# Optimization experiments

Hardware: AMD Instinct MI355X
Metric: run time of the kernel (lower is better)

The kernel has to match this reference:

```python
import jax, jax.numpy as jnp
import numpy as np

K = 16  # neighbors per point (init kwarg k)


def setup_inputs() -> dict:
    key = jax.random.key(0)
    k0, k1, k2 = jax.random.split(key, 3)
    B, N, C, L, O = 4, 8192, 32, 64, 128
    return {
        "x": jax.random.normal(k0, (B, N, C), dtype=jnp.float32),
        "W_lin": jax.random.normal(k1, (C, L), dtype=jnp.float32) * 0.1,
        "b_lin": jnp.zeros((L,), dtype=jnp.float32),
        "W_conv": jax.random.normal(k2, (L, O), dtype=jnp.float32) * 0.1,
        "b_conv": jnp.zeros((O,), dtype=jnp.float32),
    }


def reference(x, W_lin, b_lin, W_conv, b_conv):
    # --- knn(x, k): squared-euclidean pairwise distance + top-k nearest ---
    sq = jnp.sum(x * x, axis=-1)                                   # [B,N]
    # dist[b,i,j] = ||x_i - x_j||^2  (self included, dist 0)
    dist = sq[:, :, None] - 2.0 * jnp.einsum('bnc,bmc->bnm', x, x) + sq[:, None, :]
    _, idx = jax.lax.top_k(-dist, K)                               # [B,N,K] int32
    # --- index_points: gather neighbor features ---
    knn_x = jax.vmap(lambda xb, ib: xb[ib])(x, idx)                # [B,N,K,C]
    # --- max pool over neighbors ---
    pooled = jnp.max(knn_x, axis=2)                                # [B,N,C]
    # --- Dense(linear) -> Conv1D(out_channel, kernel_size=1) -> relu ---
    h = pooled @ W_lin + b_lin                                     # [B,N,64]
    h = h @ W_conv + b_conv                                        # [B,N,128]
    return jax.nn.relu(h)
```

## Files before the change

### kernel.cpp

```cpp
#include <hip/hip_runtime.h>

#define NPTS   8192
#define CCH    32
#define LDIM   64
#define ODIM   128
#define KNN    16
#define QPB    64
#define TILEC  128
#define NTIL   (NPTS / TILEC)
#define NBLK   ((4 * NPTS) / QPB)
#define SCAP   57
#define MARGIN 0.75f
#define T32STR 65

typedef _Float16 half8   __attribute__((ext_vector_type(8)));
typedef float    float4v __attribute__((ext_vector_type(4)));

#define LDS_BYTES 54016
#define OFF_SQ   8192
#define OFF_SL   34816
#define OFF_SC   49408
#define OFF_TQ   49664
#define OFF_KN   49920
#define OFF_HH   8704

__device__ __forceinline__ void gload_lds16(const void* g, void* l) {
    __builtin_amdgcn_global_load_lds(
        (const __attribute__((address_space(1))) unsigned int*)g,
        (__attribute__((address_space(3))) unsigned int*)l, 16, 0, 0);
}
__device__ __forceinline__ void gload_lds4(const void* g, void* l) {
    __builtin_amdgcn_global_load_lds(
        (const __attribute__((address_space(1))) unsigned int*)g,
        (__attribute__((address_space(3))) unsigned int*)l, 4, 0, 0);
}

__global__ void prep_kernel(const float* __restrict__ x, float* __restrict__ sqg,
                            _Float16* __restrict__ xh) {
    int p = blockIdx.x * 256 + threadIdx.x;
    const float4* src = (const float4*)(x + (size_t)p * CCH);
    float4 f[8];
    #pragma unroll
    for (int k = 0; k < 8; ++k) f[k] = src[k];
    float s = 0.f;
    #pragma unroll
    for (int k = 0; k < 8; ++k)
        s += f[k].x * f[k].x + f[k].y * f[k].y + f[k].z * f[k].z + f[k].w * f[k].w;
    sqg[p] = s;
    half8* dst = (half8*)xh + ((p >> 7) * 512 + ((p >> 4) & 7) * 64 + (p & 15));
    #pragma unroll
    for (int q = 0; q < 4; ++q) {
        float4 a = f[2 * q], c = f[2 * q + 1];
        half8 h;
        h[0] = (_Float16)a.x; h[1] = (_Float16)a.y; h[2] = (_Float16)a.z; h[3] = (_Float16)a.w;
        h[4] = (_Float16)c.x; h[5] = (_Float16)c.y; h[6] = (_Float16)c.z; h[7] = (_Float16)c.w;
        dst[q * 16] = h;
    }
}

__global__ __launch_bounds__(512, 4)
void graph_layer_kernel(const float* __restrict__ x,
                        const float* __restrict__ sqg,
                        const _Float16* __restrict__ xh,
                        const float* __restrict__ Wl,
                        const float* __restrict__ bl,
                        const float* __restrict__ Wc,
                        const float* __restrict__ bc,
                        float* __restrict__ out)
{
    __shared__ __align__(16) char smem[LDS_BYTES];
    int*   slist = (int*)(smem + OFF_SL);
    float* t32   = (float*)smem;
    int*   scnt  = (int*)(smem + OFF_SC);
    float* tq    = (float*)(smem + OFF_TQ);
    float* skeys = (float*)smem;
    int*   kn    = (int*)(smem + OFF_KN);
    float* pl    = (float*)smem;
    float* hh    = (float*)(smem + OFF_HH);

    const int tid  = threadIdx.x;
    const int lane = tid & 63;
    const int w    = tid >> 6;
    const int g    = w >> 2;
    const int lw   = w & 3;
    const int col  = lane & 15;
    const int quad = lane >> 4;
    const float INF = __builtin_inff();

    const int qb0 = blockIdx.x * QPB;
    const int b   = qb0 >> 13;
    const int qbl = qb0 & (NPTS - 1);
    const int S   = blockIdx.x & 31;
    const float* xb  = x   + (size_t)(b << 13) * CCH;
    const float* sqb = sqg + (b << 13);
    const char*  xhb = (const char*)xh + (size_t)b * NTIL * 8192;

    half8 qh;
    {
        int p = qb0 + lw * 16 + col;
        qh = *(const half8*)((const char*)xh
              + (size_t)(p >> 7) * 8192 + ((p >> 4) & 7) * 1024
              + quad * 256 + (p & 15) * 16);
    }

    auto tileof = [&](int I) { return (((I + S) & 31) << 1) | g; };
    auto bufat  = [&](int I) { return smem + (((g << 1) | (I & 1)) * 8704); };

    auto stage = [&](int I) {
        char* sb = bufat(I);
        int tile = tileof(I);
        const char* src = xhb + (size_t)tile * 8192;
        int tg = tid & 255;
        gload_lds16(src + tg * 16,        sb + lw * 1024);
        gload_lds16(src + 4096 + tg * 16, sb + 4096 + lw * 1024);
        if (lw < 2)
            gload_lds4(sqb + tile * TILEC + lw * 64 + lane, sb + OFF_SQ + lw * 256);
    };

    float m1[4] = {INF, INF, INF, INF};
    float m2[4] = {INF, INF, INF, INF};

    stage(0);
    __syncthreads();
    #pragma unroll 1
    for (int I = 0; I < 32; ++I) {
        if (I + 1 < 32) stage(I + 1);
        const char*  cb = bufat(I);
        const float* sv = (const float*)(cb + OFF_SQ);
        #pragma unroll
        for (int st = 0; st < 8; ++st) {
            half8 bh = *(const half8*)(cb + st * 1024 + lane * 16);
            float sc = sv[st * 16 + col];
            float4v acc = __builtin_amdgcn_mfma_f32_16x16x32_f16(
                qh, bh, (float4v){0.f, 0.f, 0.f, 0.f}, 0, 0, 0);
            #pragma unroll
            for (int j = 0; j < 4; ++j) {
                float key = fmaf(-2.f, acc[j], sc);
                float o1  = m1[j];
                m1[j] = fminf(key, o1);
                m2[j] = __builtin_amdgcn_fmed3f(key, o1, m2[j]);
            }
        }
        __syncthreads();
    }

    #pragma unroll
    for (int j = 0; j < 4; ++j) {
        int qq = lw * 16 + quad * 4 + j;
        t32[qq * T32STR + g * 32 + col * 2 + 0] = m1[j];
        t32[qq * T32STR + g * 32 + col * 2 + 1] = m2[j];
    }
    __syncthreads();
    {
        int q  = tid & 63;
        int wt = tid >> 6;
        float v[8]; int r[8];
        #pragma unroll
        for (int u = 0; u < 8; ++u) { v[u] = t32[q * T32STR + wt * 8 + u]; r[u] = 0; }
        #pragma unroll 8
        for (int jj = 0; jj < 64; ++jj) {
            float vj = t32[q * T32STR + jj];
            #pragma unroll
            for (int u = 0; u < 8; ++u)
                r[u] += (int)(vj < v[u]) | ((int)(vj == v[u]) & (int)(jj < wt * 8 + u));
        }
        #pragma unroll
        for (int u = 0; u < 8; ++u)
            if (r[u] == KNN - 1) tq[q] = v[u];
        if (tid < QPB) scnt[tid] = 0;
    }
    __syncthreads();
    float T2[4];
    #pragma unroll
    for (int j = 0; j < 4; ++j) T2[j] = tq[lw * 16 + quad * 4 + j] + MARGIN;

    stage(0);
    __syncthreads();
    #pragma unroll 1
    for (int I = 0; I < 32; ++I) {
        if (I + 1 < 32) stage(I + 1);
        const char*  cb = bufat(I);
        const float* sv = (const float*)(cb + OFF_SQ);
        int tbase = tileof(I) * TILEC;
        #pragma unroll
        for (int st = 0; st < 8; ++st) {
            half8 bh = *(const half8*)(cb + st * 1024 + lane * 16);
            float sc = sv[st * 16 + col];
            float4v acc = __builtin_amdgcn_mfma_f32_16x16x32_f16(
                qh, bh, (float4v){0.f, 0.f, 0.f, 0.f}, 0, 0, 0);
            #pragma unroll
            for (int j = 0; j < 4; ++j) {
                float key = fmaf(-2.f, acc[j], sc);
                if (key < T2[j]) {
                    int qq = lw * 16 + quad * 4 + j;
                    int slot = atomicAdd(&scnt[qq], 1);
                    if (slot < SCAP)
                        slist[qq * SCAP + slot] = tbase + st * 16 + col;
                }
            }
        }
        __syncthreads();
    }

    {
        int qq = tid & 63, sb8 = tid >> 6;
        int n = scnt[qq]; if (n > SCAP) n = SCAP;
        const float4* xi4 = (const float4*)(xb + (size_t)(qbl + qq) * CCH);
        for (int s = sb8; s < n; s += 8) {
            int jdx = slist[qq * SCAP + s];
            const float4* xj = (const float4*)(xb + (size_t)jdx * CCH);
            float a0 = 0.f, a1 = 0.f, a2 = 0.f, a3 = 0.f;
            #pragma unroll 2
            for (int k = 0; k < 8; ++k) {
                float4 cv = xj[k], qv = xi4[k];
                a0 = fmaf(cv.x, qv.x, a0); a1 = fmaf(cv.y, qv.y, a1);
                a2 = fmaf(cv.z, qv.z, a2); a3 = fmaf(cv.w, qv.w, a3);
            }
            float dot = (a0 + a1) + (a2 + a3);
            skeys[qq * SCAP + s] = fmaf(-2.f, dot, sqb[jdx]);
        }
    }
    __syncthreads();
    {
        int q  = tid & 63;
        int wt = tid >> 6;
        int n = scnt[q]; if (n > SCAP) n = SCAP;
        for (int s = wt; s < n; s += 8) {
            float k = skeys[q * SCAP + s];
            int   i = slist[q * SCAP + s];
            int rank = 0;
            #pragma unroll 4
            for (int jj = 0; jj < n; ++jj) {
                float kj = skeys[q * SCAP + jj];
                int   ij = slist[q * SCAP + jj];
                rank += (int)(kj < k) | ((int)(kj == k) & (int)(ij < i));
            }
            if (rank < KNN) kn[q * KNN + rank] = i;
        }
    }
    __syncthreads();

    {
        int q = tid >> 3, part = tid & 7;
        float4 m0 = make_float4(-INF, -INF, -INF, -INF);
        #pragma unroll 4
        for (int k = 0; k < KNN; ++k) {
            int j = kn[q * KNN + k];
            float4 v = *(const float4*)(xb + (size_t)j * CCH + part * 4);
            m0.x = fmaxf(m0.x, v.x); m0.y = fmaxf(m0.y, v.y);
            m0.z = fmaxf(m0.z, v.z); m0.w = fmaxf(m0.w, v.w);
        }
        float* d = pl + q * 33 + part * 4;
        d[0] = m0.x; d[1] = m0.y; d[2] = m0.z; d[3] = m0.w;
    }
    __syncthreads();
    {
        int l = tid & 63, qg2 = tid >> 6;
        #pragma unroll 1
        for (int qq = qg2; qq < QPB; qq += 8) {
            float acc = bl[l];
            #pragma unroll 8
            for (int c = 0; c < CCH; ++c)
                acc = fmaf(pl[qq * 33 + c], Wl[c * LDIM + l], acc);
            hh[qq * 65 + l] = acc;
        }
    }
    __syncthreads();
    {
        int o = tid & 127, qh2 = tid >> 7;
        #pragma unroll 1
        for (int qq = qh2; qq < QPB; qq += 4) {
            float acc = bc[o];
            #pragma unroll 8
            for (int l = 0; l < LDIM; ++l)
                acc = fmaf(hh[qq * 65 + l], Wc[l * ODIM + o], acc);
            out[(size_t)(qb0 + qq) * ODIM + o] = fmaxf(acc, 0.f);
        }
    }
}

extern "C" void kernel_launch(void* const* d_in, const int* in_sizes, int n_in,
                              void* d_out, int out_size, void* d_ws, size_t ws_size,
                              hipStream_t stream) {
    const float* x  = (const float*)d_in[0];
    const float* Wl = (const float*)d_in[1];
    const float* bl = (const float*)d_in[2];
    const float* Wc = (const float*)d_in[3];
    const float* bc = (const float*)d_in[4];
    float* out = (float*)d_out;
    float*    sqf = (float*)d_ws;
    _Float16* xh  = (_Float16*)((char*)d_ws + 131072);
    (void)in_sizes; (void)n_in; (void)out_size; (void)ws_size;

    hipLaunchKernelGGL(prep_kernel, dim3((4 * NPTS) / 256), dim3(256), 0, stream, x, sqf, xh);
    hipLaunchKernelGGL(graph_layer_kernel, dim3(NBLK), dim3(512), 0, stream,
                       x, sqf, xh, Wl, bl, Wc, bc, out);
}
```

Measured before the change: 241.2 us.

## Split kNN scan over candidate chunks and merge per-chunk top-k in finish kernel

The single fused kernel is split in two. A scan kernel gives each 64-query group four blocks, each covering a quarter of the candidate points, and writes a per-chunk top-16 list of 16-bit indices to workspace. A finish kernel merges the 64 candidates per query using exact fp32 distances, then runs the max-pool and both dense layers. The goal is many more, smaller blocks to fill the GPU better. The cost is an extra launch, a global round-trip for candidates, and recomputing exact distances for 64 candidates per query. If a chunk yields fewer than 16 survivors, unwritten candidate slots could be read.

```diff
diff --git a/kernel.cpp b/kernel.cpp
--- a/kernel.cpp
+++ b/kernel.cpp
@@ -6,23 +6,18 @@
 #define ODIM   128
 #define KNN    16
 #define QPB    64
-#define TILEC  128
-#define NTIL   (NPTS / TILEC)
-#define NBLK   ((4 * NPTS) / QPB)
-#define SCAP   57
+#define NCHK   4
+#define CHT    32
+#define SCAPC  48
 #define MARGIN 0.75f
-#define T32STR 65
 
 typedef _Float16 half8   __attribute__((ext_vector_type(8)));
 typedef float    float4v __attribute__((ext_vector_type(4)));
 
-#define LDS_BYTES 54016
-#define OFF_SQ   8192
-#define OFF_SL   34816
-#define OFF_SC   49408
-#define OFF_TQ   49664
-#define OFF_KN   49920
-#define OFF_HH   8704
+#define LDSA 18944
+#define A_SL 12288
+#define A_SC 18432
+#define A_TQ 18688
 
 __device__ __forceinline__ void gload_lds16(const void* g, void* l) {
     __builtin_amdgcn_global_load_lds(
@@ -47,7 +42,7 @@
     for (int k = 0; k < 8; ++k)
         s += f[k].x * f[k].x + f[k].y * f[k].y + f[k].z * f[k].z + f[k].w * f[k].w;
     sqg[p] = s;
-    half8* dst = (half8*)xh + ((p >> 7) * 512 + ((p >> 4) & 7) * 64 + (p & 15));
+    half8* dst = (half8*)xh + ((p >> 6) * 256 + ((p >> 4) & 3) * 64 + (p & 15));
     #pragma unroll
     for (int q = 0; q < 4; ++q) {
         float4 a = f[2 * q], c = f[2 * q + 1];
@@ -58,77 +53,62 @@
     }
 }
 
-__global__ __launch_bounds__(512, 4)
-void graph_layer_kernel(const float* __restrict__ x,
-                        const float* __restrict__ sqg,
-                        const _Float16* __restrict__ xh,
-                        const float* __restrict__ Wl,
-                        const float* __restrict__ bl,
-                        const float* __restrict__ Wc,
-                        const float* __restrict__ bc,
-                        float* __restrict__ out)
+__global__ __launch_bounds__(256, 8)
+void scan_kernel(const float* __restrict__ x,
+                 const float* __restrict__ sqg,
+                 const char* __restrict__ xh,
+                 unsigned short* __restrict__ cand)
 {
-    __shared__ __align__(16) char smem[LDS_BYTES];
-    int*   slist = (int*)(smem + OFF_SL);
-    float* t32   = (float*)smem;
-    int*   scnt  = (int*)(smem + OFF_SC);
-    float* tq    = (float*)(smem + OFF_TQ);
-    float* skeys = (float*)smem;
-    int*   kn    = (int*)(smem + OFF_KN);
-    float* pl    = (float*)smem;
-    float* hh    = (float*)(smem + OFF_HH);
+    __shared__ __align__(16) char smem[LDSA];
+    float*          t32   = (float*)smem;
+    float*          skeys = (float*)smem;
+    unsigned short* slist = (unsigned short*)(smem + A_SL);
+    int*            scnt  = (int*)(smem + A_SC);
+    float*          tq    = (float*)(smem + A_TQ);
 
     const int tid  = threadIdx.x;
     const int lane = tid & 63;
     const int w    = tid >> 6;
-    const int g    = w >> 2;
-    const int lw   = w & 3;
     const int col  = lane & 15;
     const int quad = lane >> 4;
     const float INF = __builtin_inff();
 
-    const int qb0 = blockIdx.x * QPB;
-    const int b   = qb0 >> 13;
-    const int qbl = qb0 & (NPTS - 1);
-    const int S   = blockIdx.x & 31;
+    const int chunk = blockIdx.x & (NCHK - 1);
+    const int qgi   = blockIdx.x >> 2;
+    const int qb0   = qgi * QPB;
+    const int b     = qb0 >> 13;
+    const int qbl   = qb0 & (NPTS - 1);
+    const int S     = qgi & (CHT - 1);
     const float* xb  = x   + (size_t)(b << 13) * CCH;
     const float* sqb = sqg + (b << 13);
-    const char*  xhb = (const char*)xh + (size_t)b * NTIL * 8192;
+    const char*  xhb = xh + (size_t)b * 128 * 4096;
 
     half8 qh;
     {
-        int p = qb0 + lw * 16 + col;
-        qh = *(const half8*)((const char*)xh
-              + (size_t)(p >> 7) * 8192 + ((p >> 4) & 7) * 1024
-              + quad * 256 + (p & 15) * 16);
-    }
-
-    auto tileof = [&](int I) { return (((I + S) & 31) << 1) | g; };
-    auto bufat  = [&](int I) { return smem + (((g << 1) | (I & 1)) * 8704); };
+        int p = qb0 + w * 16 + col;
+        qh = *(const half8*)(xh + (size_t)(p >> 6) * 4096 + ((p >> 4) & 3) * 1024
+                             + quad * 256 + (p & 15) * 16);
+    }
 
     auto stage = [&](int I) {
-        char* sb = bufat(I);
-        int tile = tileof(I);
-        const char* src = xhb + (size_t)tile * 8192;
-        int tg = tid & 255;
-        gload_lds16(src + tg * 16,        sb + lw * 1024);
-        gload_lds16(src + 4096 + tg * 16, sb + 4096 + lw * 1024);
-        if (lw < 2)
-            gload_lds4(sqb + tile * TILEC + lw * 64 + lane, sb + OFF_SQ + lw * 256);
+        char* sb = smem + ((I & 1) ? 4352 : 0);
+        int t = chunk * CHT + ((I + S) & (CHT - 1));
+        const char* src = xhb + (size_t)t * 4096;
+        gload_lds16(src + tid * 16, sb + w * 1024);
+        if (w == 0) gload_lds4(sqb + t * 64 + lane, sb + 4096);
     };
 
     float m1[4] = {INF, INF, INF, INF};
     float m2[4] = {INF, INF, INF, INF};
-
     stage(0);
     __syncthreads();
     #pragma unroll 1
-    for (int I = 0; I < 32; ++I) {
-        if (I + 1 < 32) stage(I + 1);
-        const char*  cb = bufat(I);
-        const float* sv = (const float*)(cb + OFF_SQ);
+    for (int I = 0; I < CHT; ++I) {
+        if (I + 1 < CHT) stage(I + 1);
+        const char*  cb = smem + ((I & 1) ? 4352 : 0);
+        const float* sv = (const float*)(cb + 4096);
         #pragma unroll
-        for (int st = 0; st < 8; ++st) {
+        for (int st = 0; st < 4; ++st) {
             half8 bh = *(const half8*)(cb + st * 1024 + lane * 16);
             float sc = sv[st * 16 + col];
             float4v acc = __builtin_amdgcn_mfma_f32_16x16x32_f16(
@@ -146,20 +126,19 @@
 
     #pragma unroll
     for (int j = 0; j < 4; ++j) {
-        int qq = lw * 16 + quad * 4 + j;
-        t32[qq * T32STR + g * 32 + col * 2 + 0] = m1[j];
-        t32[qq * T32STR + g * 32 + col * 2 + 1] = m2[j];
-    }
-    __syncthreads();
-    {
-        int q  = tid & 63;
-        int wt = tid >> 6;
+        int qq = w * 16 + quad * 4 + j;
+        t32[qq * 33 + col * 2 + 0] = m1[j];
+        t32[qq * 33 + col * 2 + 1] = m2[j];
+    }
+    __syncthreads();
+    {
+        int q = tid & 63, wt = tid >> 6;
         float v[8]; int r[8];
         #pragma unroll
-        for (int u = 0; u < 8; ++u) { v[u] = t32[q * T32STR + wt * 8 + u]; r[u] = 0; }
+        for (int u = 0; u < 8; ++u) { v[u] = t32[q * 33 + wt * 8 + u]; r[u] = 0; }
         #pragma unroll 8
-        for (int jj = 0; jj < 64; ++jj) {
-            float vj = t32[q * T32STR + jj];
+        for (int jj = 0; jj < 32; ++jj) {
+            float vj = t32[q * 33 + jj];
             #pragma unroll
             for (int u = 0; u < 8; ++u)
                 r[u] += (int)(vj < v[u]) | ((int)(vj == v[u]) & (int)(jj < wt * 8 + u));
@@ -172,18 +151,18 @@
     __syncthreads();
     float T2[4];
     #pragma unroll
-    for (int j = 0; j < 4; ++j) T2[j] = tq[lw * 16 + quad * 4 + j] + MARGIN;
+    for (int j = 0; j < 4; ++j) T2[j] = tq[w * 16 + quad * 4 + j] + MARGIN;
 
     stage(0);
     __syncthreads();
     #pragma unroll 1
-    for (int I = 0; I < 32; ++I) {
-        if (I + 1 < 32) stage(I + 1);
-        const char*  cb = bufat(I);
-        const float* sv = (const float*)(cb + OFF_SQ);
-        int tbase = tileof(I) * TILEC;
+    for (int I = 0; I < CHT; ++I) {
+        if (I + 1 < CHT) stage(I + 1);
+        const char*  cb = smem + ((I & 1) ? 4352 : 0);
+        const float* sv = (const float*)(cb + 4096);
+        int tbase = (chunk * CHT + ((I + S) & (CHT - 1))) * 64;
         #pragma unroll
-        for (int st = 0; st < 8; ++st) {
+        for (int st = 0; st < 4; ++st) {
             half8 bh = *(const half8*)(cb + st * 1024 + lane * 16);
             float sc = sv[st * 16 + col];
             float4v acc = __builtin_amdgcn_mfma_f32_16x16x32_f16(
@@ -192,10 +171,11 @@
             for (int j = 0; j < 4; ++j) {
                 float key = fmaf(-2.f, acc[j], sc);
                 if (key < T2[j]) {
-                    int qq = lw * 16 + quad * 4 + j;
+                    int qq = w * 16 + quad * 4 + j;
                     int slot = atomicAdd(&scnt[qq], 1);
-                    if (slot < SCAP)
-                        slist[qq * SCAP + slot] = tbase + st * 16 + col;
+                    if (slot < SCAPC)
+                        slist[qq * SCAPC + slot] =
+                            (unsigned short)(tbase + st * 16 + col);
                 }
             }
         }
@@ -203,11 +183,11 @@
     }
 
     {
-        int qq = tid & 63, sb8 = tid >> 6;
-        int n = scnt[qq]; if (n > SCAP) n = SCAP;
-        const float4* xi4 = (const float4*)(xb + (size_t)(qbl + qq) * CCH);
-        for (int s = sb8; s < n; s += 8) {
-            int jdx = slist[qq * SCAP + s];
+        int q = tid & 63, wt = tid >> 6;
+        int n = scnt[q]; if (n > SCAPC) n = SCAPC;
+        const float4* xi4 = (const float4*)(xb + (size_t)(qbl + q) * CCH);
+        for (int s = wt; s < n; s += 4) {
+            int jdx = slist[q * SCAPC + s];
             const float4* xj = (const float4*)(xb + (size_t)jdx * CCH);
             float a0 = 0.f, a1 = 0.f, a2 = 0.f, a3 = 0.f;
             #pragma unroll 2
@@ -217,29 +197,94 @@
                 a2 = fmaf(cv.z, qv.z, a2); a3 = fmaf(cv.w, qv.w, a3);
             }
             float dot = (a0 + a1) + (a2 + a3);
-            skeys[qq * SCAP + s] = fmaf(-2.f, dot, sqb[jdx]);
-        }
-    }
-    __syncthreads();
-    {
-        int q  = tid & 63;
-        int wt = tid >> 6;
-        int n = scnt[q]; if (n > SCAP) n = SCAP;
-        for (int s = wt; s < n; s += 8) {
-            float k = skeys[q * SCAP + s];
-            int   i = slist[q * SCAP + s];
+            skeys[q * SCAPC + s] = fmaf(-2.f, dot, sqb[jdx]);
+        }
+    }
+    __syncthreads();
+    {
+        int q = tid & 63, wt = tid >> 6;
+        int n = scnt[q]; if (n > SCAPC) n = SCAPC;
+        unsigned short* dst = cand + ((size_t)(qb0 + q) * NCHK + chunk) * KNN;
+        for (int s = wt; s < n; s += 4) {
+            float k = skeys[q * SCAPC + s];
+            int   i = slist[q * SCAPC + s];
             int rank = 0;
             #pragma unroll 4
             for (int jj = 0; jj < n; ++jj) {
-                float kj = skeys[q * SCAP + jj];
-                int   ij = slist[q * SCAP + jj];
+                float kj = skeys[q * SCAPC + jj];
+                int   ij = slist[q * SCAPC + jj];
                 rank += (int)(kj < k) | ((int)(kj == k) & (int)(ij < i));
             }
+            if (rank < KNN) dst[rank] = (unsigned short)i;
+        }
+    }
+}
+
+#define LDSB 14592
+__global__ __launch_bounds__(256, 4)
+void finish_kernel(const float* __restrict__ x,
+                   const float* __restrict__ sqg,
+                   const unsigned short* __restrict__ cand,
+                   const float* __restrict__ Wl,
+                   const float* __restrict__ bl,
+                   const float* __restrict__ Wc,
+                   const float* __restrict__ bc,
+                   float* __restrict__ out)
+{
+    __shared__ __align__(16) char smem[LDSB];
+    unsigned short* midx  = (unsigned short*)smem;
+    float*          mkeys = (float*)(smem + 4096);
+    int*            kn    = (int*)(smem + 12544);
+    float*          pl    = (float*)smem;
+    float*          hh    = (float*)(smem + 4224);
+
+    const int tid = threadIdx.x;
+    const int b   = blockIdx.x >> 8;
+    const int qbl = (blockIdx.x & 255) * 32;
+    const int qb0 = (b << 13) + qbl;
+    const float* xb  = x   + (size_t)(b << 13) * CCH;
+    const float* sqb = sqg + (b << 13);
+    const float INF = __builtin_inff();
+
+    {
+        const uint4* src = (const uint4*)(cand + (size_t)qb0 * 64);
+        ((uint4*)midx)[tid] = src[tid];
+    }
+    __syncthreads();
+    {
+        int q = tid >> 3, wt = tid & 7;
+        const float4* xi4 = (const float4*)(xb + (size_t)(qbl + q) * CCH);
+        for (int c = wt; c < 64; c += 8) {
+            int jdx = midx[q * 64 + c];
+            const float4* xj = (const float4*)(xb + (size_t)jdx * CCH);
+            float a0 = 0.f, a1 = 0.f, a2 = 0.f, a3 = 0.f;
+            #pragma unroll 2
+            for (int k = 0; k < 8; ++k) {
+                float4 cv = xj[k], qv = xi4[k];
+                a0 = fmaf(cv.x, qv.x, a0); a1 = fmaf(cv.y, qv.y, a1);
+                a2 = fmaf(cv.z, qv.z, a2); a3 = fmaf(cv.w, qv.w, a3);
+            }
+            float dot = (a0 + a1) + (a2 + a3);
+            mkeys[q * 65 + c] = fmaf(-2.f, dot, sqb[jdx]);
+        }
+    }
+    __syncthreads();
+    {
+        int q = tid >> 3, wt = tid & 7;
+        for (int c = wt; c < 64; c += 8) {
+            float k = mkeys[q * 65 + c];
+            int   i = midx[q * 64 + c];
+            int rank = 0;
+            #pragma unroll 4
+            for (int jj = 0; jj < 64; ++jj) {
+                float kj = mkeys[q * 65 + jj];
+                int   ij = midx[q * 64 + jj];
+                rank += (int)(kj < k) | ((int)(kj == k) & (int)(ij < i));
+            }
             if (rank < KNN) kn[q * KNN + rank] = i;
         }
     }
     __syncthreads();
-
     {
         int q = tid >> 3, part = tid & 7;
         float4 m0 = make_float4(-INF, -INF, -INF, -INF);
@@ -257,7 +302,7 @@
     {
         int l = tid & 63, qg2 = tid >> 6;
         #pragma unroll 1
-        for (int qq = qg2; qq < QPB; qq += 8) {
+        for (int qq = qg2; qq < 32; qq += 4) {
             float acc = bl[l];
             #pragma unroll 8
             for (int c = 0; c < CCH; ++c)
@@ -269,7 +314,7 @@
     {
         int o = tid & 127, qh2 = tid >> 7;
         #pragma unroll 1
-        for (int qq = qh2; qq < QPB; qq += 4) {
+        for (int qq = qh2; qq < 32; qq += 2) {
             float acc = bc[o];
             #pragma unroll 8
             for (int l = 0; l < LDIM; ++l)
@@ -288,11 +333,15 @@
     const float* Wc = (const float*)d_in[3];
     const float* bc = (const float*)d_in[4];
     float* out = (float*)d_out;
-    float*    sqf = (float*)d_ws;
-    _Float16* xh  = (_Float16*)((char*)d_ws + 131072);
+    float*          sqf = (float*)d_ws;
+    _Float16*       xh  = (_Float16*)((char*)d_ws + 131072);
+    unsigned short* cnd = (unsigned short*)((char*)d_ws + 131072 + 2097152);
     (void)in_sizes; (void)n_in; (void)out_size; (void)ws_size;
 
-    hipLaunchKernelGGL(prep_kernel, dim3((4 * NPTS) / 256), dim3(256), 0, stream, x, sqf, xh);
-    hipLaunchKernelGGL(graph_layer_kernel, dim3(NBLK), dim3(512), 0, stream,
-                       x, sqf, xh, Wl, bl, Wc, bc, out);
-}
+    hipLaunchKernelGGL(prep_kernel, dim3((4 * NPTS) / 256), dim3(256), 0, stream,
+                       x, sqf, xh);
+    hipLaunchKernelGGL(scan_kernel, dim3((32768 / QPB) * NCHK), dim3(256), 0, stream,
+                       x, sqf, (const char*)xh, cnd);
+    hipLaunchKernelGGL(finish_kernel, dim3(1024), dim3(256), 0, stream,
+                       x, sqf, cnd, Wl, bl, Wc, bc, out);
+}
```

After: 331.7 us. 1.38x slower.
